# Kernel tuning notes

Measured on AMD Instinct MI355X. Metric: run time of the kernel, lower is better.

The kernel has to match this reference:

```python
import jax, jax.numpy as jnp
import numpy as np

V, D, OUT, H, FF, L, K, POOL = 4097, 128, 64, 8, 256, 2, 9, 20
B, LE, LP = 32, 3000, 2000
GRID, WIDTH = 5, 257
DR = OUT // 8  # channel-attention reduction


def _ln(x, p):
    mu = jnp.mean(x, -1, keepdims=True)
    var = jnp.mean((x - mu) ** 2, -1, keepdims=True)
    return (x - mu) * jax.lax.rsqrt(var + 1e-5) * p[0] + p[1]


def _rope(x):
    # x: [B,H,S,hd], interleaved rotary embedding
    S, hd = x.shape[-2], x.shape[-1]
    inv = 1.0 / (10000.0 ** (jnp.arange(0, hd, 2, dtype=jnp.float32) / hd))
    ang = jnp.arange(S, dtype=jnp.float32)[:, None] * inv[None, :]  # [S,hd/2]
    c, s = jnp.cos(ang), jnp.sin(ang)
    x1, x2 = x[..., 0::2], x[..., 1::2]
    return jnp.stack([x1 * c - x2 * s, x1 * s + x2 * c], axis=-1).reshape(x.shape)


def _cbat_layer(x, qkv_w, qkv_b, o_w, o_b, ca_w1, ca_w2, sa_w,
                ff1_w, ff1_b, ff2_w, ff2_b, ln1, ln2):
    # x: [B,S,d] (batch-first inside CBAT, matching x.permute(1,0,2) in torch)
    Bx, S, d = x.shape
    hd = d // H

    def proj(i):
        return (x @ qkv_w[i] + qkv_b[i]).reshape(Bx, S, H, hd).transpose(0, 2, 1, 3)

    q, k, v = proj(0), proj(1), proj(2)
    q, k = _rope(q), _rope(k)
    attn = jax.nn.softmax(jnp.einsum('bhqd,bhkd->bhqk', q, k) / jnp.sqrt(jnp.float32(hd)), axis=-1)
    ctx = jnp.einsum('bhqk,bhkd->bhqd', attn, v).transpose(0, 2, 1, 3).reshape(Bx, S, d)
    # CBAM-style channel attention (pool over sequence)
    avg, mx = ctx.mean(1), ctx.max(1)  # [B,d]
    ca = jax.nn.sigmoid(jax.nn.relu(avg @ ca_w1) @ ca_w2 + jax.nn.relu(mx @ ca_w1) @ ca_w2)
    ctx = ctx * ca[:, None, :]
    # CBAM-style spatial attention (pool over channels, conv over sequence)
    feat = jnp.stack([ctx.mean(-1), ctx.max(-1)], axis=1)  # [B,2,S]
    sa = jax.nn.sigmoid(jax.lax.conv_general_dilated(
        feat, sa_w[None], (1,), 'SAME', dimension_numbers=('NCH', 'OIH', 'NCH')))  # [B,1,S]
    ctx = ctx * sa.transpose(0, 2, 1)
    out = ctx @ o_w + o_b
    aloss = jnp.mean(attn ** 2)  # adaptive attention regularizer
    x = _ln(x + out, ln1)
    ff = jax.nn.relu(x @ ff1_w + ff1_b) @ ff2_w + ff2_b
    x = _ln(x + ff, ln2)
    return x, aloss


def _mha(q_in, k_in, v_in, in_w, in_b, out_w, out_b):
    # torch nn.MultiheadAttention math (batch-first layout here; math identical)
    d = q_in.shape[-1]
    hd = d // H
    Wq, Wk, Wv = jnp.split(in_w, 3, 0)
    bq, bk, bv = jnp.split(in_b, 3, 0)

    def heads(t):
        return t.reshape(t.shape[0], t.shape[1], H, hd).transpose(0, 2, 1, 3)

    q, k, v = heads(q_in @ Wq.T + bq), heads(k_in @ Wk.T + bk), heads(v_in @ Wv.T + bv)
    attn = jax.nn.softmax(jnp.einsum('bhqd,bhkd->bhqk', q, k) / jnp.sqrt(jnp.float32(hd)), axis=-1)
    ctx = jnp.einsum('bhqk,bhkd->bhqd', attn, v).transpose(0, 2, 1, 3).reshape(q_in.shape)
    return ctx @ out_w.T + out_b


def _fourier(x, wc, ws, b):
    # FourierKAN layer: sum_k a*cos(kx) + b*sin(kx)
    kx = x[:, :, None] * jnp.arange(1, GRID + 1, dtype=x.dtype)  # [B,in,g]
    return jnp.einsum('big,oig->bo', jnp.cos(kx), wc) + jnp.einsum('big,oig->bo', jnp.sin(kx), ws) + b


def _frontend(ids, emb, conv_w, conv_b, bn):
    x = emb[ids]  # [B,Lseq,D]
    x = jax.lax.conv_general_dilated(x.transpose(0, 2, 1), conv_w, (1,), 'VALID',
                                     dimension_numbers=('NCH', 'OIH', 'NCH')) + conv_b[None, :, None]
    x = jax.nn.relu(x)
    x = jax.lax.reduce_window(x, -jnp.inf, jax.lax.max, (1, 1, POOL), (1, 1, POOL), 'VALID')
    g, be, mu, var = bn[0], bn[1], bn[2], bn[3]  # BatchNorm1d (eval mode)
    x = (x - mu[None, :, None]) * jax.lax.rsqrt(var[None, :, None] + 1e-5) * g[None, :, None] + be[None, :, None]
    return x.transpose(0, 2, 1)  # [B,S,OUT]


def _forward(enhancer_ids, promoter_ids, emb_en, emb_pr, conv_w_en, conv_b_en, conv_w_pr, conv_b_pr,
             bn_en, bn_pr, t_qkv_w, t_qkv_b, t_o_w, t_o_b, t_ca_w1, t_ca_w2, t_sa_w,
             t_ff1_w, t_ff1_b, t_ff2_w, t_ff2_b, t_ln1, t_ln2,
             cross_in_w, cross_in_b, cross_out_w, cross_out_b,
             self_in_w, self_in_b, self_out_w, self_out_b,
             fk1_c, fk1_s, fk1_b, fk2_c, fk2_s, fk2_b):
    en = _frontend(enhancer_ids, emb_en, conv_w_en, conv_b_en, bn_en)
    pr = _frontend(promoter_ids, emb_pr, conv_w_pr, conv_b_pr, bn_pr)
    total_aloss = jnp.float32(0.0)
    branches = [en, pr]
    for s in range(2):  # 0=enhancer stack, 1=promoter stack
        x = branches[s]
        for l in range(L):
            x, al = _cbat_layer(x, t_qkv_w[s, l], t_qkv_b[s, l], t_o_w[s, l], t_o_b[s, l],
                                t_ca_w1[s, l], t_ca_w2[s, l], t_sa_w[s, l],
                                t_ff1_w[s, l], t_ff1_b[s, l], t_ff2_w[s, l], t_ff2_b[s, l],
                                t_ln1[s, l], t_ln2[s, l])
            total_aloss = total_aloss + al
        branches[s] = x
    en, pr = branches
    en_att = _mha(en, pr, pr, cross_in_w, cross_in_b, cross_out_w, cross_out_b)
    en_fin = _mha(en_att, en_att, en_att, self_in_w, self_in_b, self_out_w, self_out_b)
    pr_fin = _mha(pr, pr, pr, self_in_w, self_in_b, self_out_w, self_out_b)
    combined = jnp.concatenate([en_fin.mean(1), pr_fin.mean(1)], axis=1)  # AdaptiveAvgPool1d(1)
    hidden = _fourier(combined, fk1_c, fk1_s, fk1_b)
    result = _fourier(hidden, fk2_c, fk2_s, fk2_b)
    return jax.nn.sigmoid(result), combined, total_aloss


def setup_inputs() -> dict:
    key = jax.random.key(0)
    ks = iter(jax.random.split(key, 64))

    def nrm(shape, sc=0.02):
        return jax.random.normal(next(ks), shape, jnp.float32) * sc

    ln_init = lambda: jnp.stack([jnp.ones((2, L, OUT)), jnp.zeros((2, L, OUT))], axis=2)
    inp = {
        'enhancer_ids': jax.random.randint(next(ks), (B, LE), 0, V),
        'promoter_ids': jax.random.randint(next(ks), (B, LP), 0, V),
        'enhancer_features': jax.random.normal(next(ks), (B, 10), jnp.float32),
        'promoter_features': jax.random.normal(next(ks), (B, 10), jnp.float32),
        'emb_en': nrm((V, D), 0.1), 'emb_pr': nrm((V, D), 0.1),
        'conv_w_en': nrm((OUT, D, K)), 'conv_b_en': jnp.zeros((OUT,)),
        'conv_w_pr': nrm((OUT, D, K)), 'conv_b_pr': jnp.zeros((OUT,)),
        'bn_en': jnp.stack([jnp.ones(OUT), jnp.zeros(OUT), jnp.zeros(OUT), jnp.ones(OUT)]),
        'bn_pr': jnp.stack([jnp.ones(OUT), jnp.zeros(OUT), jnp.zeros(OUT), jnp.ones(OUT)]),
        't_qkv_w': nrm((2, L, 3, OUT, OUT)), 't_qkv_b': jnp.zeros((2, L, 3, OUT)),
        't_o_w': nrm((2, L, OUT, OUT)), 't_o_b': jnp.zeros((2, L, OUT)),
        't_ca_w1': nrm((2, L, OUT, DR)), 't_ca_w2': nrm((2, L, DR, OUT)),
        't_sa_w': nrm((2, L, 2, 7)),
        't_ff1_w': nrm((2, L, OUT, FF)), 't_ff1_b': jnp.zeros((2, L, FF)),
        't_ff2_w': nrm((2, L, FF, OUT)), 't_ff2_b': jnp.zeros((2, L, OUT)),
        't_ln1': ln_init(), 't_ln2': ln_init(),
        'cross_in_w': nrm((3 * OUT, OUT)), 'cross_in_b': jnp.zeros((3 * OUT,)),
        'cross_out_w': nrm((OUT, OUT)), 'cross_out_b': jnp.zeros((OUT,)),
        'self_in_w': nrm((3 * OUT, OUT)), 'self_in_b': jnp.zeros((3 * OUT,)),
        'self_out_w': nrm((OUT, OUT)), 'self_out_b': jnp.zeros((OUT,)),
        'fk1_c': nrm((WIDTH, 2 * OUT, GRID), 0.1), 'fk1_s': nrm((WIDTH, 2 * OUT, GRID), 0.1),
        'fk1_b': jnp.zeros((WIDTH,)),
        'fk2_c': nrm((1, WIDTH, GRID), 0.1), 'fk2_s': nrm((1, WIDTH, GRID), 0.1),
        'fk2_b': jnp.zeros((1,)),
    }
    return inp


def reference(enhancer_ids, promoter_ids, enhancer_features, promoter_features,
              emb_en, emb_pr, conv_w_en, conv_b_en, conv_w_pr, conv_b_pr,
              bn_en, bn_pr, t_qkv_w, t_qkv_b, t_o_w, t_o_b, t_ca_w1, t_ca_w2, t_sa_w,
              t_ff1_w, t_ff1_b, t_ff2_w, t_ff2_b, t_ln1, t_ln2,
              cross_in_w, cross_in_b, cross_out_w, cross_out_b,
              self_in_w, self_in_b, self_out_w, self_out_b,
              fk1_c, fk1_s, fk1_b, fk2_c, fk2_s, fk2_b):
    # enhancer_features / promoter_features are accepted but unused by the original forward
    return _forward(enhancer_ids, promoter_ids, emb_en, emb_pr, conv_w_en, conv_b_en,
                    conv_w_pr, conv_b_pr, bn_en, bn_pr, t_qkv_w, t_qkv_b, t_o_w, t_o_b,
                    t_ca_w1, t_ca_w2, t_sa_w, t_ff1_w, t_ff1_b, t_ff2_w, t_ff2_b, t_ln1, t_ln2,
                    cross_in_w, cross_in_b, cross_out_w, cross_out_b,
                    self_in_w, self_in_b, self_out_w, self_out_b,
                    fk1_c, fk1_s, fk1_b, fk2_c, fk2_s, fk2_b)
```

## Files before the change

### kernel.cpp

```cpp
#include <hip/hip_runtime.h>
#include <math.h>

#define BB 32
#define SE 149
#define SP 99
#define LE_LEN 3000
#define LP_LEN 2000
#define VT 8
#define ROWS_EN (BB * SE)
#define ROWS_PR (BB * SP)
#define ROWS_ALL (ROWS_EN + ROWS_PR)

__device__ __forceinline__ void row_decode(int row, int& branch, int& b,
                                           int& s, int& S, int& lrow) {
  if (row < ROWS_EN) { branch = 0; S = SE; lrow = row; b = row / SE; s = row - b * SE; }
  else { branch = 1; S = SP; lrow = row - ROWS_EN; b = lrow / SP; s = lrow - b * SP; }
}

__global__ __launch_bounds__(256) void prep_kernel(
    const float* __restrict__ cw_en, const float* __restrict__ cw_pr,
    const float* __restrict__ cross_in, const float* __restrict__ cross_out,
    const float* __restrict__ self_in, const float* __restrict__ self_out,
    float* __restrict__ W2en, float* __restrict__ W2pr,
    float* __restrict__ Wt, float* __restrict__ Al) {
  int bb = blockIdx.x;
  if (bb == 0 && threadIdx.x == 0) Al[0] = 0.f;
  if (bb < 576) {
    const float* src = (bb < 288) ? cw_en : cw_pr;
    float* dst = (bb < 288) ? W2en : W2pr;
    int i = ((bb < 288) ? bb : bb - 288) * 256 + threadIdx.x;
    int oc = i / 1152, r = i % 1152, ic = r / 9, k = r % 9;
    dst[ic * 576 + k * 64 + oc] = src[i];
  } else {
    int m = bb - 576;
    const float* src = (m < 3) ? cross_in + m * 4096
                     : (m == 3) ? cross_out
                     : (m < 7) ? self_in + (m - 4) * 4096
                     : self_out;
    for (int i = threadIdx.x; i < 4096; i += 256) {
      int o = i >> 6, c = i & 63;
      Wt[m * 4096 + c * 64 + o] = src[i];
    }
  }
}

__global__ __launch_bounds__(192) void conv_table_kernel(
    const float* __restrict__ emb_en, const float* __restrict__ emb_pr,
    const float* __restrict__ W2en, const float* __restrict__ W2pr,
    float* __restrict__ Cen, float* __restrict__ Cpr) {
  int blk = blockIdx.x;
  int branch = (blk >= 513);
  const float* emb = branch ? emb_pr : emb_en;
  const float* W2 = branch ? W2pr : W2en;
  float* C = branch ? Cpr : Cen;
  int v0 = (branch ? blk - 513 : blk) * VT;
  __shared__ float e[VT][128];
  int t = threadIdx.x;
  int nv = 4097 - v0; if (nv > VT) nv = VT;
  for (int i = t; i < nv * 128; i += 192) e[i >> 7][i & 127] = emb[v0 * 128 + i];
  __syncthreads();
  float a0[VT], a1[VT], a2[VT];
#pragma unroll
  for (int v = 0; v < VT; ++v) { a0[v] = 0.f; a1[v] = 0.f; a2[v] = 0.f; }
  for (int ic = 0; ic < 128; ++ic) {
    float w0 = W2[ic * 576 + t];
    float w1 = W2[ic * 576 + t + 192];
    float w2 = W2[ic * 576 + t + 384];
#pragma unroll
    for (int v = 0; v < VT; ++v) {
      float ev = e[v][ic];
      a0[v] += ev * w0; a1[v] += ev * w1; a2[v] += ev * w2;
    }
  }
  for (int v = 0; v < nv; ++v) {
    C[(size_t)(v0 + v) * 576 + t] = a0[v];
    C[(size_t)(v0 + v) * 576 + t + 192] = a1[v];
    C[(size_t)(v0 + v) * 576 + t + 384] = a2[v];
  }
}

__global__ __launch_bounds__(256) void frontend_kernel(
    const int* __restrict__ en_ids, const int* __restrict__ pr_ids,
    const float* __restrict__ Cen, const float* __restrict__ Cpr,
    const float* __restrict__ cb_en, const float* __restrict__ cb_pr,
    const float* __restrict__ bn_en, const float* __restrict__ bn_pr,
    float* __restrict__ Xen, float* __restrict__ Xpr) {
  int t = threadIdx.x;
  int wid = t >> 6, oc = t & 63;
  int row = blockIdx.x * 4 + wid;
  int branch, b, s, S, lrow;
  row_decode(row, branch, b, s, S, lrow);
  const int* ids = branch ? pr_ids : en_ids;
  int Lin = branch ? LP_LEN : LE_LEN;
  const float* C = branch ? Cpr : Cen;
  const float* cb = branch ? cb_pr : cb_en;
  const float* bn = branch ? bn_pr : bn_en;
  float* X = branch ? Xpr : Xen;
  __shared__ int idl[4][28];
  if (oc < 28) idl[wid][oc] = ids[b * Lin + s * 20 + oc];
  __syncthreads();
  float bias = cb[oc];
  float m = -INFINITY;
  for (int p = 0; p < 20; ++p) {
    float acc = bias;
#pragma unroll
    for (int k = 0; k < 9; ++k) acc += C[idl[wid][p + k] * 576 + k * 64 + oc];
    acc = fmaxf(acc, 0.f);
    m = fmaxf(m, acc);
  }
  float g = bn[oc], be = bn[64 + oc], mu = bn[128 + oc], var = bn[192 + oc];
  X[(size_t)lrow * 64 + oc] = (m - mu) * rsqrtf(var + 1e-5f) * g + be;
}

__global__ __launch_bounds__(256) void qkv_rope_kernel(
    const float* __restrict__ Xen, const float* __restrict__ Xpr,
    const float* __restrict__ t_qkv_w, const float* __restrict__ t_qkv_b, int l,
    float* __restrict__ Q, float* __restrict__ K, float* __restrict__ V) {
  int t = threadIdx.x;
  int wid = t >> 6, oc = t & 63;
  int row = blockIdx.x * 4 + wid;
  int branch, b, s, S, lrow;
  row_decode(row, branch, b, s, S, lrow);
  const float* X = branch ? Xpr : Xen;
  int idx = branch * 2 + l;
  const float* W = t_qkv_w + (size_t)idx * 3 * 4096;
  const float* bias = t_qkv_b + idx * 192;
  __shared__ float xr[4][64], qs[4][64], ks[4][64];
  xr[wid][oc] = X[lrow * 64 + oc];
  __syncthreads();
  float q0 = bias[oc], k0 = bias[64 + oc], v0 = bias[128 + oc];
  float q1 = 0.f, k1 = 0.f, v1 = 0.f;
  for (int c = 0; c < 64; c += 2) {
    float xa = xr[wid][c], xb = xr[wid][c + 1];
    q0 += xa * W[c * 64 + oc];
    q1 += xb * W[(c + 1) * 64 + oc];
    k0 += xa * W[4096 + c * 64 + oc];
    k1 += xb * W[4096 + (c + 1) * 64 + oc];
    v0 += xa * W[8192 + c * 64 + oc];
    v1 += xb * W[8192 + (c + 1) * 64 + oc];
  }
  float q = q0 + q1, k = k0 + k1, v = v0 + v1;
  qs[wid][oc] = q; ks[wid][oc] = k;
  V[row * 64 + oc] = v;
  __syncthreads();
  int j = oc & 7;
  int p = j >> 1;
  float inv = powf(10000.f, -(float)p * 0.25f);
  float ang = (float)s * inv;
  float cc = cosf(ang), ss = sinf(ang);
  float qo, ko;
  if ((j & 1) == 0) {
    qo = qs[wid][oc] * cc - qs[wid][oc + 1] * ss;
    ko = ks[wid][oc] * cc - ks[wid][oc + 1] * ss;
  } else {
    qo = qs[wid][oc - 1] * ss + qs[wid][oc] * cc;
    ko = ks[wid][oc - 1] * ss + ks[wid][oc] * cc;
  }
  Q[row * 64 + oc] = qo;
  K[row * 64 + oc] = ko;
}

__global__ __launch_bounds__(640) void attn_kernel(
    const float* __restrict__ Q, const float* __restrict__ K,
    const float* __restrict__ V, float* __restrict__ ctx,
    int nblk0, int Sq0, int Sk0, int qb0, int kb0, float als0,
    int Sq1, int Sk1, int qb1, int kb1, float als1,
    float* __restrict__ aloss_acc) {
  int blk = blockIdx.x;
  int bh, Sq, Sk, qb, kb; float als;
  if (blk < nblk0) { bh = blk; Sq = Sq0; Sk = Sk0; qb = qb0; kb = kb0; als = als0; }
  else { bh = blk - nblk0; Sq = Sq1; Sk = Sk1; qb = qb1; kb = kb1; als = als1; }
  int b = bh >> 3, h = bh & 7;
  __shared__ float kk[160 * 8], vv[160 * 8];
  __shared__ float pm[3][160], psum[3][160], psum2[3][160], pacc[3][160][8];
  int t = threadIdx.x;
  int g = t / 160, tq = t - g * 160;
  for (int i = t; i < Sk * 2; i += 640) {
    int r = i >> 1, j = i & 1;
    const float4* ksrc = (const float4*)(K + (size_t)(kb + b * Sk + r) * 64 + h * 8);
    const float4* vsrc = (const float4*)(V + (size_t)(kb + b * Sk + r) * 64 + h * 8);
    ((float4*)kk)[i] = ksrc[j];
    ((float4*)vv)[i] = vsrc[j];
  }
  __syncthreads();
  int quarter = (Sk + 3) >> 2;
  int kbeg = g * quarter;
  int kend = kbeg + quarter; if (kend > Sk) kend = Sk;
  float m = -INFINITY, sum = 0.f, sum2 = 0.f, acc[8];
#pragma unroll
  for (int j = 0; j < 8; ++j) acc[j] = 0.f;
  if (tq < Sq) {
    float q[8];
#pragma unroll
    for (int j = 0; j < 8; ++j) q[j] = Q[(size_t)(qb + b * Sq + tq) * 64 + h * 8 + j];
    const float sc = 0.35355339059327373f;
    for (int kki = kbeg; kki < kend; ++kki) {
      float sdot = 0.f;
#pragma unroll
      for (int j = 0; j < 8; ++j) sdot += q[j] * kk[kki * 8 + j];
      sdot *= sc;
      if (sdot > m) {
        float f = __expf(m - sdot);
        sum *= f; sum2 *= f * f;
#pragma unroll
        for (int j = 0; j < 8; ++j) acc[j] *= f;
        m = sdot;
      }
      float e = __expf(sdot - m);
      sum += e; sum2 += e * e;
#pragma unroll
      for (int j = 0; j < 8; ++j) acc[j] += e * vv[kki * 8 + j];
    }
  }
  if (g > 0 && tq < Sq) {
    pm[g - 1][tq] = m; psum[g - 1][tq] = sum; psum2[g - 1][tq] = sum2;
#pragma unroll
    for (int j = 0; j < 8; ++j) pacc[g - 1][tq][j] = acc[j];
  }
  __syncthreads();
  float rowsum2 = 0.f;
  if (g == 0 && tq < Sq) {
    float mf = m;
#pragma unroll
    for (int p = 0; p < 3; ++p) mf = fmaxf(mf, pm[p][tq]);
    float f0 = __expf(m - mf);
    float f1 = __expf(pm[0][tq] - mf);
    float f2 = __expf(pm[1][tq] - mf);
    float f3 = __expf(pm[2][tq] - mf);
    float sumf = sum * f0 + psum[0][tq] * f1 + psum[1][tq] * f2 + psum[2][tq] * f3;
    float invs = 1.f / sumf;
#pragma unroll
    for (int j = 0; j < 8; ++j) {
      float a = acc[j] * f0 + pacc[0][tq][j] * f1 + pacc[1][tq][j] * f2 +
                pacc[2][tq][j] * f3;
      ctx[(size_t)(qb + b * Sq + tq) * 64 + h * 8 + j] = a * invs;
    }
    rowsum2 = (sum2 * f0 * f0 + psum2[0][tq] * f1 * f1 +
               psum2[1][tq] * f2 * f2 + psum2[2][tq] * f3 * f3) * invs * invs;
  }
  if (als != 0.f) {
    float wsum = rowsum2;
    for (int off = 32; off; off >>= 1) wsum += __shfl_down(wsum, off, 64);
    __shared__ float wred[10];
    if ((t & 63) == 0) wred[t >> 6] = wsum;
    __syncthreads();
    if (t == 0) {
      float tot = 0.f;
#pragma unroll
      for (int w = 0; w < 10; ++w) tot += wred[w];
      atomicAdd(aloss_acc, tot * als);
    }
  }
}

__global__ __launch_bounds__(512) void ca_kernel(
    const float* __restrict__ ctx, const float* __restrict__ t_ca_w1,
    const float* __restrict__ t_ca_w2, int l, float* __restrict__ ca) {
  int bp = blockIdx.x;
  int branch = bp >> 5, b = bp & 31;
  int S = branch ? SP : SE;
  int base = branch ? ROWS_EN : 0;
  int idx = branch * 2 + l;
  const float* W1 = t_ca_w1 + idx * 512;
  const float* W2 = t_ca_w2 + idx * 512;
  int t = threadIdx.x;
  int c = t & 63, seg = t >> 6;
  float sum = 0.f, mx = -INFINITY;
  for (int s = seg; s < S; s += 8) {
    float v = ctx[(size_t)(base + b * S + s) * 64 + c];
    sum += v; mx = fmaxf(mx, v);
  }
  __shared__ float ssum[8][64], smx[8][64];
  ssum[seg][c] = sum; smx[seg][c] = mx;
  __syncthreads();
  __shared__ float avg_l[64], mx_l[64], ha[8], hm[8];
  if (t < 64) {
    float a = 0.f, m = -INFINITY;
#pragma unroll
    for (int g = 0; g < 8; ++g) { a += ssum[g][t]; m = fmaxf(m, smx[g][t]); }
    avg_l[t] = a / (float)S; mx_l[t] = m;
  }
  __syncthreads();
  if (t < 8) {
    float a = 0.f, m2 = 0.f;
    for (int i = 0; i < 64; ++i) {
      a += avg_l[i] * W1[i * 8 + t];
      m2 += mx_l[i] * W1[i * 8 + t];
    }
    ha[t] = fmaxf(a, 0.f); hm[t] = fmaxf(m2, 0.f);
  }
  __syncthreads();
  if (t < 64) {
    float o = 0.f;
#pragma unroll
    for (int j = 0; j < 8; ++j) o += (ha[j] + hm[j]) * W2[j * 64 + t];
    ca[bp * 64 + t] = 1.f / (1.f + expf(-o));
  }
}

__global__ __launch_bounds__(256) void feat_kernel(
    float* __restrict__ ctx, const float* __restrict__ ca,
    float* __restrict__ fmean, float* __restrict__ fmax) {
  int row = blockIdx.x * 4 + (threadIdx.x >> 6);
  int branch, b, s, S, lrow;
  row_decode(row, branch, b, s, S, lrow);
  int c = threadIdx.x & 63;
  float v = ctx[row * 64 + c] * ca[(branch * 32 + b) * 64 + c];
  ctx[row * 64 + c] = v;
  float sum = v, mx = v;
  for (int off = 32; off; off >>= 1) {
    sum += __shfl_xor(sum, off, 64);
    mx = fmaxf(mx, __shfl_xor(mx, off, 64));
  }
  if (c == 0) { fmean[row] = sum * (1.f / 64.f); fmax[row] = mx; }
}

__global__ __launch_bounds__(256) void tail_kernel(
    const float* __restrict__ ctx, const float* __restrict__ fmean,
    const float* __restrict__ fmax, const float* __restrict__ t_sa_w,
    const float* __restrict__ t_o_w, const float* __restrict__ t_o_b,
    const float* __restrict__ t_ln1, const float* __restrict__ t_ff1_w,
    const float* __restrict__ t_ff1_b, const float* __restrict__ t_ff2_w,
    const float* __restrict__ t_ff2_b, const float* __restrict__ t_ln2,
    int l, float* __restrict__ Xen, float* __restrict__ Xpr) {
  int t = threadIdx.x;
  int wid = t >> 6, lane = t & 63;
  int row = blockIdx.x * 4 + wid;
  int branch, b, s, S, lrow;
  row_decode(row, branch, b, s, S, lrow);
  int idx = branch * 2 + l;
  const float* sa_w = t_sa_w + idx * 14;
  float sa = 0.f;
  if (lane == 0) {
    for (int k = 0; k < 7; ++k) {
      int p = s + k - 3;
      if (p >= 0 && p < S)
        sa += fmean[row - s + p] * sa_w[k] + fmax[row - s + p] * sa_w[7 + k];
    }
    sa = 1.f / (1.f + expf(-sa));
  }
  sa = __shfl(sa, 0, 64);
  __shared__ float rowv[4][64], xr[4][64], h[4][256];
  rowv[wid][lane] = ctx[row * 64 + lane] * sa;
  __syncthreads();
  const float* o_w = t_o_w + (size_t)idx * 4096;
  float p0 = t_o_b[idx * 64 + lane], p1 = 0.f, p2 = 0.f, p3 = 0.f;
  for (int c = 0; c < 64; c += 4) {
    p0 += rowv[wid][c] * o_w[c * 64 + lane];
    p1 += rowv[wid][c + 1] * o_w[(c + 1) * 64 + lane];
    p2 += rowv[wid][c + 2] * o_w[(c + 2) * 64 + lane];
    p3 += rowv[wid][c + 3] * o_w[(c + 3) * 64 + lane];
  }
  float o = (p0 + p1) + (p2 + p3);
  float* X = branch ? Xpr : Xen;
  float r = X[lrow * 64 + lane] + o;
  float mu = r;
  for (int of = 32; of; of >>= 1) mu += __shfl_xor(mu, of, 64);
  mu *= (1.f / 64.f);
  float d = r - mu;
  float var = d * d;
  for (int of = 32; of; of >>= 1) var += __shfl_xor(var, of, 64);
  var *= (1.f / 64.f);
  const float* ln1 = t_ln1 + idx * 128;
  float x1 = d * rsqrtf(var + 1e-5f) * ln1[lane] + ln1[64 + lane];
  xr[wid][lane] = x1;
  __syncthreads();
  const float* W1 = t_ff1_w + (size_t)idx * 16384;
  float a0 = t_ff1_b[idx * 256 + t], a1 = a0, a2 = a0, a3 = a0;
  for (int c = 0; c < 64; ++c) {
    float w = W1[c * 256 + t];
    a0 += xr[0][c] * w; a1 += xr[1][c] * w; a2 += xr[2][c] * w; a3 += xr[3][c] * w;
  }
  h[0][t] = fmaxf(a0, 0.f); h[1][t] = fmaxf(a1, 0.f);
  h[2][t] = fmaxf(a2, 0.f); h[3][t] = fmaxf(a3, 0.f);
  __syncthreads();
  const float* W2 = t_ff2_w + (size_t)idx * 16384;
  float q0 = t_ff2_b[idx * 64 + lane], q1 = 0.f, q2 = 0.f, q3 = 0.f;
  for (int j = 0; j < 256; j += 4) {
    q0 += h[wid][j] * W2[j * 64 + lane];
    q1 += h[wid][j + 1] * W2[(j + 1) * 64 + lane];
    q2 += h[wid][j + 2] * W2[(j + 2) * 64 + lane];
    q3 += h[wid][j + 3] * W2[(j + 3) * 64 + lane];
  }
  float o2 = (q0 + q1) + (q2 + q3);
  float r2 = x1 + o2;
  mu = r2;
  for (int of = 32; of; of >>= 1) mu += __shfl_xor(mu, of, 64);
  mu *= (1.f / 64.f);
  d = r2 - mu;
  var = d * d;
  for (int of = 32; of; of >>= 1) var += __shfl_xor(var, of, 64);
  var *= (1.f / 64.f);
  const float* ln2 = t_ln2 + idx * 128;
  X[lrow * 64 + lane] = d * rsqrtf(var + 1e-5f) * ln2[lane] + ln2[64 + lane];
}

__global__ __launch_bounds__(256) void cross_proj_kernel(
    const float* __restrict__ Xen, const float* __restrict__ Xpr,
    const float* __restrict__ Wt, const float* __restrict__ bias,
    float* __restrict__ Q, float* __restrict__ K, float* __restrict__ V) {
  int t = threadIdx.x;
  int wid = t >> 6, oc = t & 63;
  int blk = blockIdx.x;
  __shared__ float xr[4][64];
  if (blk < ROWS_EN / 4) {
    int row = blk * 4 + wid;
    xr[wid][oc] = Xen[row * 64 + oc];
    __syncthreads();
    float p0 = bias[oc], p1 = 0.f, p2 = 0.f, p3 = 0.f;
    for (int c = 0; c < 64; c += 4) {
      p0 += xr[wid][c] * Wt[c * 64 + oc];
      p1 += xr[wid][c + 1] * Wt[(c + 1) * 64 + oc];
      p2 += xr[wid][c + 2] * Wt[(c + 2) * 64 + oc];
      p3 += xr[wid][c + 3] * Wt[(c + 3) * 64 + oc];
    }
    Q[row * 64 + oc] = (p0 + p1) + (p2 + p3);
  } else {
    int lr = (blk - ROWS_EN / 4) * 4 + wid;
    xr[wid][oc] = Xpr[lr * 64 + oc];
    __syncthreads();
    float k0 = bias[64 + oc], k1 = 0.f, v0 = bias[128 + oc], v1 = 0.f;
    for (int c = 0; c < 64; c += 2) {
      float xa = xr[wid][c], xb = xr[wid][c + 1];
      k0 += xa * Wt[4096 + c * 64 + oc];
      k1 += xb * Wt[4096 + (c + 1) * 64 + oc];
      v0 += xa * Wt[8192 + c * 64 + oc];
      v1 += xb * Wt[8192 + (c + 1) * 64 + oc];
    }
    K[(ROWS_EN + lr) * 64 + oc] = k0 + k1;
    V[(ROWS_EN + lr) * 64 + oc] = v0 + v1;
  }
}

__global__ __launch_bounds__(256) void self_qkv_kernel(
    const float* __restrict__ inEn, const float* __restrict__ inPr,
    const float* __restrict__ Wt, const float* __restrict__ bias,
    float* __restrict__ Q, float* __restrict__ K, float* __restrict__ V) {
  int t = threadIdx.x;
  int wid = t >> 6, oc = t & 63;
  int row = blockIdx.x * 4 + wid;
  const float* in; int lrow;
  if (row < ROWS_EN) { in = inEn; lrow = row; }
  else { in = inPr; lrow = row - ROWS_EN; }
  __shared__ float xr[4][64];
  xr[wid][oc] = in[lrow * 64 + oc];
  __syncthreads();
  float q0 = bias[oc], k0 = bias[64 + oc], v0 = bias[128 + oc];
  float q1 = 0.f, k1 = 0.f, v1 = 0.f;
  for (int c = 0; c < 64; c += 2) {
    float xa = xr[wid][c], xb = xr[wid][c + 1];
    q0 += xa * Wt[c * 64 + oc];
    q1 += xb * Wt[(c + 1) * 64 + oc];
    k0 += xa * Wt[4096 + c * 64 + oc];
    k1 += xb * Wt[4096 + (c + 1) * 64 + oc];
    v0 += xa * Wt[8192 + c * 64 + oc];
    v1 += xb * Wt[8192 + (c + 1) * 64 + oc];
  }
  Q[row * 64 + oc] = q0 + q1;
  K[row * 64 + oc] = k0 + k1;
  V[row * 64 + oc] = v0 + v1;
}

__global__ __launch_bounds__(256) void dual_proj_kernel(
    const float* __restrict__ in, const float* __restrict__ Wt,
    const float* __restrict__ bias, float* __restrict__ out0,
    float* __restrict__ out1) {
  int t = threadIdx.x;
  int wid = t >> 6, oc = t & 63;
  int row = blockIdx.x * 4 + wid;
  float* out; int lrow;
  if (row < ROWS_EN) { out = out0; lrow = row; }
  else { out = out1; lrow = row - ROWS_EN; }
  __shared__ float xr[4][64];
  xr[wid][oc] = in[row * 64 + oc];
  __syncthreads();
  float p0 = bias[oc], p1 = 0.f, p2 = 0.f, p3 = 0.f;
  for (int c = 0; c < 64; c += 4) {
    p0 += xr[wid][c] * Wt[c * 64 + oc];
    p1 += xr[wid][c + 1] * Wt[(c + 1) * 64 + oc];
    p2 += xr[wid][c + 2] * Wt[(c + 2) * 64 + oc];
    p3 += xr[wid][c + 3] * Wt[(c + 3) * 64 + oc];
  }
  out[lrow * 64 + oc] = (p0 + p1) + (p2 + p3);
}

__global__ __launch_bounds__(512) void mean_trig_kernel(
    const float* __restrict__ en_fin, const float* __restrict__ pr_fin,
    float* __restrict__ comb, float* __restrict__ trig) {
  int b = blockIdx.x;
  int t = threadIdx.x;
  int col = t & 127, seg = t >> 7;
  float sum = 0.f;
  if (col < 64) {
    for (int s = seg; s < SE; s += 4) sum += en_fin[(b * SE + s) * 64 + col];
  } else {
    int c = col - 64;
    for (int s = seg; s < SP; s += 4) sum += pr_fin[(b * SP + s) * 64 + c];
  }
  __shared__ float red[4][128];
  __shared__ float comb_s[128];
  red[seg][col] = sum;
  __syncthreads();
  if (t < 128) {
    float tot = red[0][t] + red[1][t] + red[2][t] + red[3][t];
    float cv = tot / (t < 64 ? (float)SE : (float)SP);
    comb_s[t] = cv;
    comb[b * 128 + t] = cv;
  }
  __syncthreads();
  for (int i = t; i < 640; i += 512) {
    int ii = i / 5, g = i - ii * 5;
    float x = comb_s[ii] * (float)(g + 1);
    trig[b * 1280 + i] = cosf(x);
    trig[b * 1280 + 640 + i] = sinf(x);
  }
}

__global__ __launch_bounds__(256) void fourier1_kernel(
    const float* __restrict__ trig, const float* __restrict__ wc,
    const float* __restrict__ ws, const float* __restrict__ bias,
    float* __restrict__ hidden) {
  int b = blockIdx.x;
  int t = threadIdx.x;
  int wid = t >> 6, lane = t & 63;
  int o = blockIdx.y * 4 + wid;
  if (o >= 257) return;
  const float* ct = trig + b * 1280;
  const float* st = ct + 640;
  float acc = 0.f;
  for (int i = lane; i < 640; i += 64)
    acc += ct[i] * wc[(size_t)o * 640 + i] + st[i] * ws[(size_t)o * 640 + i];
  for (int off = 32; off; off >>= 1) acc += __shfl_xor(acc, off, 64);
  if (lane == 0) hidden[b * 257 + o] = acc + bias[o];
}

__global__ void fourier2_kernel(const float* __restrict__ hidden,
                                const float* __restrict__ wc,
                                const float* __restrict__ ws,
                                const float* __restrict__ bias,
                                const float* __restrict__ aloss_acc,
                                float* __restrict__ out) {
  int b = blockIdx.x;
  int t = threadIdx.x;
  float acc = 0.f;
  if (t < 257) {
    float x = hidden[b * 257 + t];
#pragma unroll
    for (int g = 0; g < 5; ++g) {
      float a = x * (float)(g + 1);
      acc += cosf(a) * wc[t * 5 + g] + sinf(a) * ws[t * 5 + g];
    }
  }
  for (int off = 32; off; off >>= 1) acc += __shfl_xor(acc, off, 64);
  __shared__ float wred[5];
  if ((t & 63) == 0) wred[t >> 6] = acc;
  __syncthreads();
  if (t == 0) {
    float tot = wred[0] + wred[1] + wred[2] + wred[3] + wred[4] + bias[0];
    out[b] = 1.f / (1.f + expf(-tot));
    if (b == 0) out[4128] = aloss_acc[0];
  }
}

extern "C" void kernel_launch(void* const* d_in, const int* in_sizes, int n_in,
                              void* d_out, int out_size, void* d_ws, size_t ws_size,
                              hipStream_t stream) {
  const int* en_ids = (const int*)d_in[0];
  const int* pr_ids = (const int*)d_in[1];
  const float* emb_en = (const float*)d_in[4];
  const float* emb_pr = (const float*)d_in[5];
  const float* conv_w_en = (const float*)d_in[6];
  const float* conv_b_en = (const float*)d_in[7];
  const float* conv_w_pr = (const float*)d_in[8];
  const float* conv_b_pr = (const float*)d_in[9];
  const float* bn_en = (const float*)d_in[10];
  const float* bn_pr = (const float*)d_in[11];
  const float* t_qkv_w = (const float*)d_in[12];
  const float* t_qkv_b = (const float*)d_in[13];
  const float* t_o_w = (const float*)d_in[14];
  const float* t_o_b = (const float*)d_in[15];
  const float* t_ca_w1 = (const float*)d_in[16];
  const float* t_ca_w2 = (const float*)d_in[17];
  const float* t_sa_w = (const float*)d_in[18];
  const float* t_ff1_w = (const float*)d_in[19];
  const float* t_ff1_b = (const float*)d_in[20];
  const float* t_ff2_w = (const float*)d_in[21];
  const float* t_ff2_b = (const float*)d_in[22];
  const float* t_ln1 = (const float*)d_in[23];
  const float* t_ln2 = (const float*)d_in[24];
  const float* cross_in_w = (const float*)d_in[25];
  const float* cross_in_b = (const float*)d_in[26];
  const float* cross_out_w = (const float*)d_in[27];
  const float* cross_out_b = (const float*)d_in[28];
  const float* self_in_w = (const float*)d_in[29];
  const float* self_in_b = (const float*)d_in[30];
  const float* self_out_w = (const float*)d_in[31];
  const float* self_out_b = (const float*)d_in[32];
  const float* fk1_c = (const float*)d_in[33];
  const float* fk1_s = (const float*)d_in[34];
  const float* fk1_b = (const float*)d_in[35];
  const float* fk2_c = (const float*)d_in[36];
  const float* fk2_s = (const float*)d_in[37];
  const float* fk2_b = (const float*)d_in[38];

  float* out = (float*)d_out;
  float* ws = (float*)d_ws;
  size_t off = 0;
  float* Cen = ws + off;  off += (size_t)4097 * 576;
  float* Cpr = ws + off;  off += (size_t)4097 * 576;
  float* W2en = ws + off; off += 73728;
  float* W2pr = ws + off; off += 73728;
  float* Wt = ws + off;   off += 8 * 4096;
  float* Xen = ws + off;  off += (size_t)ROWS_EN * 64;
  float* Xpr = ws + off;  off += (size_t)ROWS_PR * 64;
  float* Qb = ws + off;   off += (size_t)ROWS_ALL * 64;
  float* Kb = ws + off;   off += (size_t)ROWS_ALL * 64;
  float* Vb = ws + off;   off += (size_t)ROWS_ALL * 64;
  float* Ctx = ws + off;  off += (size_t)ROWS_ALL * 64;
  float* AttEn = ws + off; off += (size_t)ROWS_EN * 64;
  float* PrFin = ws + off; off += (size_t)ROWS_PR * 64;
  float* Fm = ws + off;   off += ROWS_ALL;
  float* Fx = ws + off;   off += ROWS_ALL;
  float* CaB = ws + off;  off += 2 * BB * 64;
  float* Hid = ws + off;  off += BB * 257;
  float* Trig = ws + off; off += (size_t)BB * 1280;
  float* Al = ws + off;   off += 8;

  const float als_en = 1.f / ((float)BB * 8.f * (float)SE * (float)SE);
  const float als_pr = 1.f / ((float)BB * 8.f * (float)SP * (float)SP);

  prep_kernel<<<584, 256, 0, stream>>>(conv_w_en, conv_w_pr, cross_in_w,
                                       cross_out_w, self_in_w, self_out_w,
                                       W2en, W2pr, Wt, Al);
  conv_table_kernel<<<1026, 192, 0, stream>>>(emb_en, emb_pr, W2en, W2pr, Cen, Cpr);
  frontend_kernel<<<ROWS_ALL / 4, 256, 0, stream>>>(en_ids, pr_ids, Cen, Cpr,
                                                    conv_b_en, conv_b_pr, bn_en,
                                                    bn_pr, Xen, Xpr);

  for (int l = 0; l < 2; ++l) {
    qkv_rope_kernel<<<ROWS_ALL / 4, 256, 0, stream>>>(Xen, Xpr, t_qkv_w,
                                                      t_qkv_b, l, Qb, Kb, Vb);
    attn_kernel<<<512, 640, 0, stream>>>(Qb, Kb, Vb, Ctx,
                                         256, SE, SE, 0, 0, als_en,
                                         SP, SP, ROWS_EN, ROWS_EN, als_pr, Al);
    ca_kernel<<<64, 512, 0, stream>>>(Ctx, t_ca_w1, t_ca_w2, l, CaB);
    feat_kernel<<<ROWS_ALL / 4, 256, 0, stream>>>(Ctx, CaB, Fm, Fx);
    tail_kernel<<<ROWS_ALL / 4, 256, 0, stream>>>(
        Ctx, Fm, Fx, t_sa_w, t_o_w, t_o_b, t_ln1, t_ff1_w, t_ff1_b,
        t_ff2_w, t_ff2_b, t_ln2, l, Xen, Xpr);
  }

  cross_proj_kernel<<<ROWS_ALL / 4, 256, 0, stream>>>(Xen, Xpr, Wt,
                                                      cross_in_b, Qb, Kb, Vb);
  attn_kernel<<<256, 640, 0, stream>>>(Qb, Kb, Vb, Ctx,
                                       256, SE, SP, 0, ROWS_EN, 0.f,
                                       0, 0, 0, 0, 0.f, Al);
  dual_proj_kernel<<<ROWS_EN / 4, 256, 0, stream>>>(Ctx, Wt + 3 * 4096,
                                                    cross_out_b, AttEn, AttEn);

  self_qkv_kernel<<<ROWS_ALL / 4, 256, 0, stream>>>(AttEn, Xpr, Wt + 4 * 4096,
                                                    self_in_b, Qb, Kb, Vb);
  attn_kernel<<<512, 640, 0, stream>>>(Qb, Kb, Vb, Ctx,
                                       256, SE, SE, 0, 0, 0.f,
                                       SP, SP, ROWS_EN, ROWS_EN, 0.f, Al);
  dual_proj_kernel<<<ROWS_ALL / 4, 256, 0, stream>>>(Ctx, Wt + 7 * 4096,
                                                     self_out_b, Xen, PrFin);

  mean_trig_kernel<<<BB, 512, 0, stream>>>(Xen, PrFin, out + 32, Trig);
  fourier1_kernel<<<dim3(BB, 65), 256, 0, stream>>>(Trig, fk1_c, fk1_s,
                                                    fk1_b, Hid);
  fourier2_kernel<<<BB, 320, 0, stream>>>(Hid, fk2_c, fk2_s, fk2_b, Al, out);
}
```

Before: 313.5 us.

## Fuse channel-attention apply into ca kernel and widen tail kernel to 8 rows

Merges the feat_kernel into the channel-attention kernel, so each per-batch block computes the channel gate, applies it to ctx, and emits the per-row mean and max, which removes one launch and the CaB round trip. The tail kernel now processes 8 rows per 512-thread block instead of 4, reusing each weight load across more rows. The trade-off is that the fused stage runs on only 64 blocks, so the elementwise pass loses parallelism, and the larger tail block raises shared memory and register pressure.

```diff
diff --git a/kernel.cpp b/kernel.cpp
--- a/kernel.cpp
+++ b/kernel.cpp
@@ -253,9 +253,10 @@
   }
 }
 
-__global__ __launch_bounds__(512) void ca_kernel(
-    const float* __restrict__ ctx, const float* __restrict__ t_ca_w1,
-    const float* __restrict__ t_ca_w2, int l, float* __restrict__ ca) {
+__global__ __launch_bounds__(512) void cafeat_kernel(
+    float* __restrict__ ctx, const float* __restrict__ t_ca_w1,
+    const float* __restrict__ t_ca_w2, int l,
+    float* __restrict__ fmean, float* __restrict__ fmax) {
   int bp = blockIdx.x;
   int branch = bp >> 5, b = bp & 31;
   int S = branch ? SP : SE;
@@ -273,7 +274,7 @@
   __shared__ float ssum[8][64], smx[8][64];
   ssum[seg][c] = sum; smx[seg][c] = mx;
   __syncthreads();
-  __shared__ float avg_l[64], mx_l[64], ha[8], hm[8];
+  __shared__ float avg_l[64], mx_l[64], ha[8], hm[8], ca_s[64];
   if (t < 64) {
     float a = 0.f, m = -INFINITY;
 #pragma unroll
@@ -294,28 +295,24 @@
     float o = 0.f;
 #pragma unroll
     for (int j = 0; j < 8; ++j) o += (ha[j] + hm[j]) * W2[j * 64 + t];
-    ca[bp * 64 + t] = 1.f / (1.f + expf(-o));
-  }
-}
-
-__global__ __launch_bounds__(256) void feat_kernel(
-    float* __restrict__ ctx, const float* __restrict__ ca,
-    float* __restrict__ fmean, float* __restrict__ fmax) {
-  int row = blockIdx.x * 4 + (threadIdx.x >> 6);
-  int branch, b, s, S, lrow;
-  row_decode(row, branch, b, s, S, lrow);
-  int c = threadIdx.x & 63;
-  float v = ctx[row * 64 + c] * ca[(branch * 32 + b) * 64 + c];
-  ctx[row * 64 + c] = v;
-  float sum = v, mx = v;
-  for (int off = 32; off; off >>= 1) {
-    sum += __shfl_xor(sum, off, 64);
-    mx = fmaxf(mx, __shfl_xor(mx, off, 64));
-  }
-  if (c == 0) { fmean[row] = sum * (1.f / 64.f); fmax[row] = mx; }
-}
-
-__global__ __launch_bounds__(256) void tail_kernel(
+    ca_s[t] = 1.f / (1.f + expf(-o));
+  }
+  __syncthreads();
+  float cav = ca_s[c];
+  for (int s = seg; s < S; s += 8) {
+    int grow = base + b * S + s;
+    float v = ctx[(size_t)grow * 64 + c] * cav;
+    ctx[(size_t)grow * 64 + c] = v;
+    float su = v, mv = v;
+    for (int off = 32; off; off >>= 1) {
+      su += __shfl_xor(su, off, 64);
+      mv = fmaxf(mv, __shfl_xor(mv, off, 64));
+    }
+    if (c == 0) { fmean[grow] = su * (1.f / 64.f); fmax[grow] = mv; }
+  }
+}
+
+__global__ __launch_bounds__(512) void tail_kernel(
     const float* __restrict__ ctx, const float* __restrict__ fmean,
     const float* __restrict__ fmax, const float* __restrict__ t_sa_w,
     const float* __restrict__ t_o_w, const float* __restrict__ t_o_b,
@@ -325,7 +322,7 @@
     int l, float* __restrict__ Xen, float* __restrict__ Xpr) {
   int t = threadIdx.x;
   int wid = t >> 6, lane = t & 63;
-  int row = blockIdx.x * 4 + wid;
+  int row = blockIdx.x * 8 + wid;
   int branch, b, s, S, lrow;
   row_decode(row, branch, b, s, S, lrow);
   int idx = branch * 2 + l;
@@ -340,8 +337,8 @@
     sa = 1.f / (1.f + expf(-sa));
   }
   sa = __shfl(sa, 0, 64);
-  __shared__ float rowv[4][64], xr[4][64], h[4][256];
-  rowv[wid][lane] = ctx[row * 64 + lane] * sa;
+  __shared__ float rowv[8][64], xr[8][64], h[8][256];
+  rowv[wid][lane] = ctx[(size_t)row * 64 + lane] * sa;
   __syncthreads();
   const float* o_w = t_o_w + (size_t)idx * 4096;
   float p0 = t_o_b[idx * 64 + lane], p1 = 0.f, p2 = 0.f, p3 = 0.f;
@@ -353,7 +350,7 @@
   }
   float o = (p0 + p1) + (p2 + p3);
   float* X = branch ? Xpr : Xen;
-  float r = X[lrow * 64 + lane] + o;
+  float r = X[(size_t)lrow * 64 + lane] + o;
   float mu = r;
   for (int of = 32; of; of >>= 1) mu += __shfl_xor(mu, of, 64);
   mu *= (1.f / 64.f);
@@ -366,13 +363,18 @@
   xr[wid][lane] = x1;
   __syncthreads();
   const float* W1 = t_ff1_w + (size_t)idx * 16384;
-  float a0 = t_ff1_b[idx * 256 + t], a1 = a0, a2 = a0, a3 = a0;
-  for (int c = 0; c < 64; ++c) {
-    float w = W1[c * 256 + t];
-    a0 += xr[0][c] * w; a1 += xr[1][c] * w; a2 += xr[2][c] * w; a3 += xr[3][c] * w;
-  }
-  h[0][t] = fmaxf(a0, 0.f); h[1][t] = fmaxf(a1, 0.f);
-  h[2][t] = fmaxf(a2, 0.f); h[3][t] = fmaxf(a3, 0.f);
+  {
+    int jcol = t & 255;
+    int rg = (t >> 8) * 4;
+    float a0 = t_ff1_b[idx * 256 + jcol], a1 = a0, a2 = a0, a3 = a0;
+    for (int c = 0; c < 64; ++c) {
+      float w = W1[c * 256 + jcol];
+      a0 += xr[rg + 0][c] * w; a1 += xr[rg + 1][c] * w;
+      a2 += xr[rg + 2][c] * w; a3 += xr[rg + 3][c] * w;
+    }
+    h[rg + 0][jcol] = fmaxf(a0, 0.f); h[rg + 1][jcol] = fmaxf(a1, 0.f);
+    h[rg + 2][jcol] = fmaxf(a2, 0.f); h[rg + 3][jcol] = fmaxf(a3, 0.f);
+  }
   __syncthreads();
   const float* W2 = t_ff2_w + (size_t)idx * 16384;
   float q0 = t_ff2_b[idx * 64 + lane], q1 = 0.f, q2 = 0.f, q3 = 0.f;
@@ -392,7 +394,7 @@
   for (int of = 32; of; of >>= 1) var += __shfl_xor(var, of, 64);
   var *= (1.f / 64.f);
   const float* ln2 = t_ln2 + idx * 128;
-  X[lrow * 64 + lane] = d * rsqrtf(var + 1e-5f) * ln2[lane] + ln2[64 + lane];
+  X[(size_t)lrow * 64 + lane] = d * rsqrtf(var + 1e-5f) * ln2[lane] + ln2[64 + lane];
 }
 
 __global__ __launch_bounds__(256) void cross_proj_kernel(
@@ -621,7 +623,6 @@
   float* PrFin = ws + off; off += (size_t)ROWS_PR * 64;
   float* Fm = ws + off;   off += ROWS_ALL;
   float* Fx = ws + off;   off += ROWS_ALL;
-  float* CaB = ws + off;  off += 2 * BB * 64;
   float* Hid = ws + off;  off += BB * 257;
   float* Trig = ws + off; off += (size_t)BB * 1280;
   float* Al = ws + off;   off += 8;
@@ -643,9 +644,8 @@
     attn_kernel<<<512, 640, 0, stream>>>(Qb, Kb, Vb, Ctx,
                                          256, SE, SE, 0, 0, als_en,
                                          SP, SP, ROWS_EN, ROWS_EN, als_pr, Al);
-    ca_kernel<<<64, 512, 0, stream>>>(Ctx, t_ca_w1, t_ca_w2, l, CaB);
-    feat_kernel<<<ROWS_ALL / 4, 256, 0, stream>>>(Ctx, CaB, Fm, Fx);
-    tail_kernel<<<ROWS_ALL / 4, 256, 0, stream>>>(
+    cafeat_kernel<<<64, 512, 0, stream>>>(Ctx, t_ca_w1, t_ca_w2, l, Fm, Fx);
+    tail_kernel<<<ROWS_ALL / 8, 512, 0, stream>>>(
         Ctx, Fm, Fx, t_sa_w, t_o_w, t_o_b, t_ln1, t_ff1_w, t_ff1_b,
         t_ff2_w, t_ff2_b, t_ln2, l, Xen, Xpr);
   }
```

After: 322.9 us. 1.03x slower.
